# Kernel tuning notes

Hardware: AMD Instinct MI355X
Metric: run time of the kernel (lower is better)

## Reference

```python
import jax, jax.numpy as jnp
import numpy as np

B, S, D = 2, 2048, 2048
H = 16
HD = D // H  # 128


def setup_inputs() -> dict:
    key = jax.random.key(0)
    ks = jax.random.split(key, 9)
    s = 1.0 / np.sqrt(D)
    return {
        "hidden_states": jax.random.normal(ks[0], (B, S, D), dtype=jnp.float32),
        "Wq": jax.random.normal(ks[1], (D, D), dtype=jnp.float32) * s,
        "bq": jnp.zeros((D,), dtype=jnp.float32),
        "Wk": jax.random.normal(ks[2], (D, D), dtype=jnp.float32) * s,
        "bk": jnp.zeros((D,), dtype=jnp.float32),
        "Wv": jax.random.normal(ks[3], (D, D), dtype=jnp.float32) * s,
        "bv": jnp.zeros((D,), dtype=jnp.float32),
        "Wo": jax.random.normal(ks[4], (D, D), dtype=jnp.float32) * s,
        "bo": jnp.zeros((D,), dtype=jnp.float32),
    }


def reference(hidden_states, Wq, bq, Wk, bk, Wv, bv, Wo, bo):
    x = hidden_states
    # linear projections (torch Linear: x @ W.T + b)
    q = x @ Wq.T + bq
    k = x @ Wk.T + bk
    v = x @ Wv.T + bv
    # [B, S, H, HD] -> [B, H, S, HD]
    q = q.reshape(B, S, H, HD).transpose(0, 2, 1, 3)
    k = k.reshape(B, S, H, HD).transpose(0, 2, 1, 3)
    v = v.reshape(B, S, H, HD).transpose(0, 2, 1, 3)
    q = q / jnp.sqrt(jnp.float32(HD))
    # scores [B, H, S, S]
    scores = jnp.einsum("bhqd,bhkd->bhqk", q, k)
    causal = jnp.triu(jnp.full((S, S), -jnp.inf, dtype=scores.dtype), k=1)
    scores = scores + causal
    attn = jax.nn.softmax(scores, axis=-1)
    out = jnp.einsum("bhqk,bhkd->bhqd", attn, v)
    out = out.transpose(0, 2, 1, 3).reshape(B, S, D)
    return out @ Wo.T + bo
```

## Files before the change

### kernel.cpp

```cpp
#include <hip/hip_runtime.h>
#include <stdint.h>

#define S_LEN 2048
#define DMODEL 2048
#define NHEAD 16
#define HDIM 128

typedef __attribute__((ext_vector_type(8))) short short8;
typedef __attribute__((ext_vector_type(4))) float floatx4;

__device__ __forceinline__ unsigned short f2b(float f) {
  union { float f; unsigned u; } v; v.f = f;
  unsigned r = v.u + 0x7FFFu + ((v.u >> 16) & 1u);
  return (unsigned short)(r >> 16);
}

__device__ __forceinline__ void load_lds16(const unsigned short* g, unsigned short* l) {
  __builtin_amdgcn_global_load_lds((const __attribute__((address_space(1))) void*)g,
                                   (__attribute__((address_space(3))) void*)l, 16, 0, 0);
}

__global__ __launch_bounds__(256) void cvt_all(const float* __restrict__ x,
                                               const float* __restrict__ Wq, const float* __restrict__ Wk,
                                               const float* __restrict__ Wv, const float* __restrict__ Wo,
                                               unsigned short* __restrict__ xb,
                                               unsigned short* __restrict__ Wqb, unsigned short* __restrict__ Wkb,
                                               unsigned short* __restrict__ Wvb, unsigned short* __restrict__ Wob) {
  const size_t idx = (size_t)blockIdx.x * 256 + threadIdx.x;
  const int y = blockIdx.y;
  const float4* s; ushort4* d;
  if (y == 0)      { s = (const float4*)x;               d = (ushort4*)xb; }
  else if (y == 1) { s = (const float4*)x + (1u << 20);  d = (ushort4*)xb + (1u << 20); }
  else if (y == 2) { s = (const float4*)Wq;              d = (ushort4*)Wqb; }
  else if (y == 3) { s = (const float4*)Wk;              d = (ushort4*)Wkb; }
  else if (y == 4) { s = (const float4*)Wv;              d = (ushort4*)Wvb; }
  else             { s = (const float4*)Wo;              d = (ushort4*)Wob; }
  float4 f = s[idx];
  ushort4 o;
  o.x = f2b(f.x); o.y = f2b(f.y); o.z = f2b(f.z); o.w = f2b(f.w);
  d[idx] = o;
}

template <int MODE>
__global__ __launch_bounds__(256)
void gemm_bt(const unsigned short* __restrict__ A, const unsigned short* __restrict__ Bw,
             const float* __restrict__ bias, void* __restrict__ Cout,
             int M, int N, int K, float scale) {
  __shared__ unsigned short As[128 * 64];
  __shared__ unsigned short Bs[128 * 64];
  const int t = threadIdx.x;
  const int lane = t & 63, wave = t >> 6;
  const int quad = lane >> 4, lc = lane & 15;
  const int wm = wave >> 1, wn = wave & 1;
  const int m0 = blockIdx.y * 128, n0 = blockIdx.x * 128;

  const int srow = lane >> 3;
  const int skoff = ((lane & 7) ^ srow) * 8;
  const unsigned short* Ag[4];
  const unsigned short* Bg[4];
  unsigned short* Al[4];
  unsigned short* Bl[4];
#pragma unroll
  for (int i = 0; i < 4; i++) {
    int c = wave * 4 + i;
    Ag[i] = A + (size_t)(m0 + c * 8 + srow) * K + skoff;
    Bg[i] = Bw + (size_t)(n0 + c * 8 + srow) * K + skoff;
    Al[i] = &As[c * 512 + lane * 8];
    Bl[i] = &Bs[c * 512 + lane * 8];
  }

  int koff[2];
#pragma unroll
  for (int ks = 0; ks < 2; ks++) koff[ks] = ((ks * 4 + quad) ^ (lc & 7)) * 8;

  floatx4 acc[4][4] = {};

  for (int kt = 0; kt < K; kt += 64) {
    if (kt) __syncthreads();
#pragma unroll
    for (int i = 0; i < 4; i++) {
      load_lds16(Ag[i] + kt, Al[i]);
      load_lds16(Bg[i] + kt, Bl[i]);
    }
    __syncthreads();
#pragma unroll
    for (int ks = 0; ks < 2; ks++) {
      short8 av[4], bv[4];
#pragma unroll
      for (int mt = 0; mt < 4; mt++)
        av[mt] = *(const short8*)&As[(wm * 64 + mt * 16 + lc) * 64 + koff[ks]];
#pragma unroll
      for (int nt = 0; nt < 4; nt++)
        bv[nt] = *(const short8*)&Bs[(wn * 64 + nt * 16 + lc) * 64 + koff[ks]];
#pragma unroll
      for (int mt = 0; mt < 4; mt++)
#pragma unroll
        for (int nt = 0; nt < 4; nt++)
          acc[mt][nt] = __builtin_amdgcn_mfma_f32_16x16x32_bf16(av[mt], bv[nt], acc[mt][nt], 0, 0, 0);
    }
  }

#pragma unroll
  for (int nt = 0; nt < 4; nt++) {
    const int col = n0 + wn * 64 + nt * 16 + lc;
    const float bcol = bias[col];
#pragma unroll
    for (int mt = 0; mt < 4; mt++) {
      const int row0 = m0 + wm * 64 + mt * 16 + quad * 4;
      if (MODE == 1) {
        ushort4 o;
        o.x = f2b((acc[mt][nt][0] + bcol) * scale);
        o.y = f2b((acc[mt][nt][1] + bcol) * scale);
        o.z = f2b((acc[mt][nt][2] + bcol) * scale);
        o.w = f2b((acc[mt][nt][3] + bcol) * scale);
        int b = row0 >> 11;
        int s = row0 & (S_LEN - 1);
        *(ushort4*)&((unsigned short*)Cout)[((size_t)(b * DMODEL + col)) * S_LEN + s] = o;
      } else {
#pragma unroll
        for (int r = 0; r < 4; r++) {
          float v = (acc[mt][nt][r] + bcol) * scale;
          if (MODE == 2)
            ((float*)Cout)[(size_t)(row0 + r) * N + col] = v;
          else
            ((unsigned short*)Cout)[(size_t)(row0 + r) * N + col] = f2b(v);
        }
      }
    }
  }
}

__global__ __launch_bounds__(256, 2)
void attn_fwd(const unsigned short* __restrict__ Qg, const unsigned short* __restrict__ Kg,
              const unsigned short* __restrict__ Vtg, unsigned short* __restrict__ Og) {
  __shared__ unsigned short Ks[2][64 * 128];
  __shared__ unsigned short Vs[128 * 64];
  __shared__ unsigned short Ps[128 * 72];

  const int t = threadIdx.x;
  const int lane = t & 63, w = t >> 6;
  const int quad = lane >> 4, lc = lane & 15;
  const int y = blockIdx.y;
  const int tile = (y < 16) ? (int)blockIdx.x : 15 - (int)blockIdx.x;
  const int b = y >> 4, h = y & 15;
  const size_t qkbase = (size_t)b * S_LEN * DMODEL + h * HDIM;
  const size_t vtbase = ((size_t)(b * DMODEL + h * HDIM)) * S_LEN;
  const int q0 = tile * 128;
  const int wrow = q0 + w * 32;

  short8 aq[2][4];
#pragma unroll
  for (int pm = 0; pm < 2; pm++)
#pragma unroll
    for (int ks = 0; ks < 4; ks++)
      aq[pm][ks] = *(const short8*)&Qg[qkbase + (size_t)(wrow + pm * 16 + lc) * DMODEL + ks * 32 + quad * 8];

  const unsigned short* kga[4];
  const unsigned short* vga[4];
  int kloff[4], vloff[4];
#pragma unroll
  for (int i = 0; i < 4; i++) {
    int c = w * 4 + i;
    int krow = 4 * c + (lane >> 4);
    kga[i] = Kg + qkbase + (size_t)krow * DMODEL + ((lane & 15) ^ (krow & 15)) * 8;
    kloff[i] = c * 512 + lane * 8;
    int vrow = 8 * c + (lane >> 3);
    vga[i] = Vtg + vtbase + (size_t)vrow * S_LEN + ((lane & 7) ^ (vrow & 7)) * 8;
    vloff[i] = c * 512 + lane * 8;
  }

  floatx4 oaccT[8][2] = {};
  float m_run[2] = {-1e30f, -1e30f}, l_run[2] = {0.f, 0.f};

  const int kiters = 2 * tile + 2;

#pragma unroll
  for (int i = 0; i < 4; i++) load_lds16(kga[i], &Ks[0][kloff[i]]);

  for (int kb = 0; kb < kiters; kb++) {
    const int k0 = kb * 64;
    const int cur = kb & 1;
    __syncthreads();

#pragma unroll
    for (int i = 0; i < 4; i++) load_lds16(vga[i] + k0, &Vs[vloff[i]]);
    {
      const size_t knext = (size_t)((kb + 1 < kiters) ? k0 + 64 : k0) * DMODEL;
#pragma unroll
      for (int i = 0; i < 4; i++) load_lds16(kga[i] + knext, &Ks[cur ^ 1][kloff[i]]);
    }

    const bool hasw = (k0 <= wrow + 31);
    float alpha[2];
    if (hasw) {
      floatx4 st[4][2];
#pragma unroll
      for (int mt = 0; mt < 4; mt++)
#pragma unroll
        for (int pm = 0; pm < 2; pm++) st[mt][pm] = (floatx4){0.f, 0.f, 0.f, 0.f};
#pragma unroll
      for (int ks = 0; ks < 4; ks++) {
        short8 kf[4];
#pragma unroll
        for (int mt = 0; mt < 4; mt++) {
          int n = mt * 16 + lc;
          kf[mt] = *(const short8*)&Ks[cur][n * 128 + (((ks * 4 + quad) ^ (n & 15)) * 8)];
        }
#pragma unroll
        for (int mt = 0; mt < 4; mt++)
#pragma unroll
          for (int pm = 0; pm < 2; pm++)
            st[mt][pm] = __builtin_amdgcn_mfma_f32_16x16x32_bf16(kf[mt], aq[pm][ks], st[mt][pm], 0, 0, 0);
      }

      float mx[2] = {-1e30f, -1e30f};
      if (k0 + 63 > wrow) {
#pragma unroll
        for (int pm = 0; pm < 2; pm++) {
          const int qq = wrow + pm * 16 + lc;
#pragma unroll
          for (int mt = 0; mt < 4; mt++) {
            const int key = k0 + mt * 16 + quad * 4;
#pragma unroll
            for (int r = 0; r < 4; r++) {
              if (key + r > qq) st[mt][pm][r] = -1e30f;
              mx[pm] = fmaxf(mx[pm], st[mt][pm][r]);
            }
          }
        }
      } else {
#pragma unroll
        for (int pm = 0; pm < 2; pm++)
#pragma unroll
          for (int mt = 0; mt < 4; mt++)
#pragma unroll
            for (int r = 0; r < 4; r++) mx[pm] = fmaxf(mx[pm], st[mt][pm][r]);
      }
#pragma unroll
      for (int pm = 0; pm < 2; pm++) {
        mx[pm] = fmaxf(mx[pm], __shfl_xor(mx[pm], 16));
        mx[pm] = fmaxf(mx[pm], __shfl_xor(mx[pm], 32));
        float mnew = fmaxf(m_run[pm], mx[pm]);
        alpha[pm] = __builtin_amdgcn_exp2f(m_run[pm] - mnew);
        m_run[pm] = mnew;
        l_run[pm] *= alpha[pm];
      }

#pragma unroll
      for (int pm = 0; pm < 2; pm++)
#pragma unroll
        for (int mt = 0; mt < 4; mt++) {
          float p0 = __builtin_amdgcn_exp2f(st[mt][pm][0] - m_run[pm]);
          float p1 = __builtin_amdgcn_exp2f(st[mt][pm][1] - m_run[pm]);
          float p2 = __builtin_amdgcn_exp2f(st[mt][pm][2] - m_run[pm]);
          float p3 = __builtin_amdgcn_exp2f(st[mt][pm][3] - m_run[pm]);
          l_run[pm] += (p0 + p1) + (p2 + p3);
          ushort4 o;
          o.x = f2b(p0); o.y = f2b(p1); o.z = f2b(p2); o.w = f2b(p3);
          *(ushort4*)&Ps[(w * 32 + pm * 16 + lc) * 72 + mt * 16 + quad * 4] = o;
        }
    }

    asm volatile("s_waitcnt vmcnt(4)\n\ts_barrier" ::: "memory");

    if (hasw) {
#pragma unroll
      for (int mt8 = 0; mt8 < 8; mt8++)
#pragma unroll
        for (int pm = 0; pm < 2; pm++) {
          oaccT[mt8][pm][0] *= alpha[pm]; oaccT[mt8][pm][1] *= alpha[pm];
          oaccT[mt8][pm][2] *= alpha[pm]; oaccT[mt8][pm][3] *= alpha[pm];
        }

#pragma unroll
      for (int ks = 0; ks < 2; ks++) {
        short8 pf[2];
#pragma unroll
        for (int pm = 0; pm < 2; pm++)
          pf[pm] = *(const short8*)&Ps[(w * 32 + pm * 16 + lc) * 72 + ks * 32 + quad * 8];
#pragma unroll
        for (int mt8 = 0; mt8 < 8; mt8++) {
          int n = mt8 * 16 + lc;
          short8 vf = *(const short8*)&Vs[n * 64 + (((ks * 4 + quad) ^ (n & 7)) * 8)];
#pragma unroll
          for (int pm = 0; pm < 2; pm++)
            oaccT[mt8][pm] = __builtin_amdgcn_mfma_f32_16x16x32_bf16(vf, pf[pm], oaccT[mt8][pm], 0, 0, 0);
        }
      }
    }
  }

#pragma unroll
  for (int pm = 0; pm < 2; pm++) {
    l_run[pm] += __shfl_xor(l_run[pm], 16);
    l_run[pm] += __shfl_xor(l_run[pm], 32);
    float inv = 1.f / l_run[pm];
    size_t obase = ((size_t)(b * S_LEN + wrow + pm * 16 + lc)) * DMODEL + h * HDIM;
#pragma unroll
    for (int mt8 = 0; mt8 < 8; mt8++) {
      ushort4 o;
      o.x = f2b(oaccT[mt8][pm][0] * inv);
      o.y = f2b(oaccT[mt8][pm][1] * inv);
      o.z = f2b(oaccT[mt8][pm][2] * inv);
      o.w = f2b(oaccT[mt8][pm][3] * inv);
      *(ushort4*)&Og[obase + mt8 * 16 + quad * 4] = o;
    }
  }
}

extern "C" void kernel_launch(void* const* d_in, const int* in_sizes, int n_in,
                              void* d_out, int out_size, void* d_ws, size_t ws_size,
                              hipStream_t stream) {
  const float* x  = (const float*)d_in[0];
  const float* Wq = (const float*)d_in[1];
  const float* bq = (const float*)d_in[2];
  const float* Wk = (const float*)d_in[3];
  const float* bk = (const float*)d_in[4];
  const float* Wv = (const float*)d_in[5];
  const float* bv = (const float*)d_in[6];
  const float* Wo = (const float*)d_in[7];
  const float* bo = (const float*)d_in[8];

  const int M = 2 * S_LEN;
  const int N = DMODEL, K = DMODEL;

  char* w = (char*)d_ws;
  unsigned short* xb  = (unsigned short*)(w);
  unsigned short* Wqb = (unsigned short*)(w + (size_t)16 * (1 << 20));
  unsigned short* Wkb = (unsigned short*)(w + (size_t)24 * (1 << 20));
  unsigned short* Wvb = (unsigned short*)(w + (size_t)32 * (1 << 20));
  unsigned short* Wob = (unsigned short*)(w + (size_t)40 * (1 << 20));
  unsigned short* Qb  = (unsigned short*)(w + (size_t)48 * (1 << 20));
  unsigned short* Kb  = (unsigned short*)(w + (size_t)64 * (1 << 20));
  unsigned short* Vtb = (unsigned short*)(w + (size_t)80 * (1 << 20));
  unsigned short* Ob  = (unsigned short*)(w + (size_t)96 * (1 << 20));

  cvt_all<<<dim3(4096, 6), 256, 0, stream>>>(x, Wq, Wk, Wv, Wo, xb, Wqb, Wkb, Wvb, Wob);

  dim3 gg(N / 128, M / 128);
  const float qscale = 0.08838834764831843f * 1.4426950408889634f;
  gemm_bt<0><<<gg, 256, 0, stream>>>(xb, Wqb, bq, Qb, M, N, K, qscale);
  gemm_bt<0><<<gg, 256, 0, stream>>>(xb, Wkb, bk, Kb, M, N, K, 1.f);
  gemm_bt<1><<<gg, 256, 0, stream>>>(xb, Wvb, bv, Vtb, M, N, K, 1.f);

  attn_fwd<<<dim3(16, 32), 256, 0, stream>>>(Qb, Kb, Vtb, Ob);

  gemm_bt<2><<<gg, 256, 0, stream>>>(Ob, Wob, bo, d_out, M, N, K, 1.f);
}
```

Baseline: 380.8 us.

## Replace GEMMs with 256x256 pipelined LDS kernel and fuse QKV launches

Replaces the 128x128 single-buffered GEMM with a 256x256-tile, 512-thread kernel that double-buffers K slices in LDS via async global-to-LDS loads. Explicit vmcnt/lgkmcnt waits, barriers and priority hints interleave loads with MFMA clusters. The Q, K and V projections are merged into one launch selecting the weight by block index. Larger tiles raise arithmetic intensity and hide load latency, but the output GEMM now has only 128 blocks and the 128KB LDS per block limits occupancy.

```diff
diff --git a/kernel.cpp b/kernel.cpp
--- a/kernel.cpp
+++ b/kernel.cpp
@@ -41,93 +41,137 @@
   d[idx] = o;
 }
 
-template <int MODE>
-__global__ __launch_bounds__(256)
-void gemm_bt(const unsigned short* __restrict__ A, const unsigned short* __restrict__ Bw,
-             const float* __restrict__ bias, void* __restrict__ Cout,
-             int M, int N, int K, float scale) {
-  __shared__ unsigned short As[128 * 64];
-  __shared__ unsigned short Bs[128 * 64];
+
+#define REG256(buf, op, ks) (lds + ((((buf)*2 + (op)) * 2 + (ks)) * 8192))
+#define STAGE256(buf, op, ks, kt)                                                    \
+  do {                                                                               \
+    unsigned short* _d = REG256(buf, op, ks);                                        \
+    const unsigned short* _g0 = ((op) ? gB[0] : gA[0]) + (kt) * 64 + (ks) * 32;      \
+    const unsigned short* _g1 = ((op) ? gB[1] : gA[1]) + (kt) * 64 + (ks) * 32;      \
+    load_lds16(_g0, _d + ldso[0]);                                                   \
+    load_lds16(_g1, _d + ldso[1]);                                                   \
+  } while (0)
+#define RDA256(buf, ks)                                                              \
+  { _Pragma("unroll") for (int mf = 0; mf < 8; mf++)                                 \
+      av[mf] = *(const short8*)(REG256(buf, 0, ks) + aoff + mf * 512); }
+#define RDB256(buf, ks, nh)                                                          \
+  { bv[0] = *(const short8*)(REG256(buf, 1, ks) + boff + (nh) * 1024);               \
+    bv[1] = *(const short8*)(REG256(buf, 1, ks) + boff + (nh) * 1024 + 512); }
+#define MFMACL256(nh)                                                                \
+  { __builtin_amdgcn_s_setprio(1);                                                   \
+    _Pragma("unroll") for (int mf = 0; mf < 8; mf++) {                               \
+      acc[mf][(nh)*2]   = __builtin_amdgcn_mfma_f32_16x16x32_bf16(av[mf], bv[0], acc[mf][(nh)*2],   0, 0, 0); \
+      acc[mf][(nh)*2+1] = __builtin_amdgcn_mfma_f32_16x16x32_bf16(av[mf], bv[1], acc[mf][(nh)*2+1], 0, 0, 0); } \
+    __builtin_amdgcn_s_setprio(0); }
+#define BAR256 __builtin_amdgcn_s_barrier()
+#define LGKM0 do { asm volatile("s_waitcnt lgkmcnt(0)" ::: "memory"); __builtin_amdgcn_sched_barrier(0); } while (0)
+#define VMC4 asm volatile("s_waitcnt vmcnt(4)" ::: "memory")
+
+__device__ __forceinline__ void gemm256_body(const unsigned short* __restrict__ A,
+                                             const unsigned short* __restrict__ Bw,
+                                             const float* __restrict__ bias,
+                                             void* __restrict__ out, int mode, float scale,
+                                             int m0, int n0, unsigned short* lds) {
+  const int K = DMODEL;
   const int t = threadIdx.x;
-  const int lane = t & 63, wave = t >> 6;
+  const int lane = t & 63, w = t >> 6;
   const int quad = lane >> 4, lc = lane & 15;
-  const int wm = wave >> 1, wn = wave & 1;
-  const int m0 = blockIdx.y * 128, n0 = blockIdx.x * 128;
-
-  const int srow = lane >> 3;
-  const int skoff = ((lane & 7) ^ srow) * 8;
-  const unsigned short* Ag[4];
-  const unsigned short* Bg[4];
-  unsigned short* Al[4];
-  unsigned short* Bl[4];
-#pragma unroll
-  for (int i = 0; i < 4; i++) {
-    int c = wave * 4 + i;
-    Ag[i] = A + (size_t)(m0 + c * 8 + srow) * K + skoff;
-    Bg[i] = Bw + (size_t)(n0 + c * 8 + srow) * K + skoff;
-    Al[i] = &As[c * 512 + lane * 8];
-    Bl[i] = &Bs[c * 512 + lane * 8];
-  }
-
-  int koff[2];
-#pragma unroll
-  for (int ks = 0; ks < 2; ks++) koff[ks] = ((ks * 4 + quad) ^ (lc & 7)) * 8;
-
-  floatx4 acc[4][4] = {};
-
-  for (int kt = 0; kt < K; kt += 64) {
-    if (kt) __syncthreads();
-#pragma unroll
-    for (int i = 0; i < 4; i++) {
-      load_lds16(Ag[i] + kt, Al[i]);
-      load_lds16(Bg[i] + kt, Bl[i]);
-    }
-    __syncthreads();
-#pragma unroll
-    for (int ks = 0; ks < 2; ks++) {
-      short8 av[4], bv[4];
-#pragma unroll
-      for (int mt = 0; mt < 4; mt++)
-        av[mt] = *(const short8*)&As[(wm * 64 + mt * 16 + lc) * 64 + koff[ks]];
-#pragma unroll
-      for (int nt = 0; nt < 4; nt++)
-        bv[nt] = *(const short8*)&Bs[(wn * 64 + nt * 16 + lc) * 64 + koff[ks]];
-#pragma unroll
-      for (int mt = 0; mt < 4; mt++)
-#pragma unroll
-        for (int nt = 0; nt < 4; nt++)
-          acc[mt][nt] = __builtin_amdgcn_mfma_f32_16x16x32_bf16(av[mt], bv[nt], acc[mt][nt], 0, 0, 0);
-    }
-  }
-
-#pragma unroll
-  for (int nt = 0; nt < 4; nt++) {
-    const int col = n0 + wn * 64 + nt * 16 + lc;
+  const int wm = w >> 2, wn = w & 3;
+
+  const int chunkoff = ((lane & 3) ^ ((lane >> 3) & 3)) * 8;
+  const unsigned short* gA[2];
+  const unsigned short* gB[2];
+  int ldso[2];
+#pragma unroll
+  for (int i = 0; i < 2; i++) {
+    const int c = w * 2 + i;
+    const int r = c * 16 + (lane >> 2);
+    gA[i] = A + (size_t)(m0 + r) * K + chunkoff;
+    gB[i] = Bw + (size_t)(n0 + r) * K + chunkoff;
+    ldso[i] = c * 512 + lane * 8;
+  }
+
+  const int rsw = ((lc >> 1) & 3);
+  const int aoff = (wm * 128 + lc) * 32 + ((quad ^ rsw) * 8);
+  const int boff = (wn * 64 + lc) * 32 + ((quad ^ rsw) * 8);
+
+  floatx4 acc[8][4] = {};
+  short8 av[8], bv[2];
+
+  STAGE256(0, 0, 0, 0); STAGE256(0, 1, 0, 0); STAGE256(0, 0, 1, 0); STAGE256(0, 1, 1, 0);
+  STAGE256(1, 0, 0, 1); STAGE256(1, 1, 0, 1);
+  VMC4;
+  BAR256;
+
+  const int NKT = K / 64;
+  const int NIT = NKT / 2;
+  for (int it = 0; it < NIT; it++) {
+    const int kt1 = 2 * it + 1;
+    const int kt2 = (2 * it + 2 < NKT) ? 2 * it + 2 : NKT - 1;
+    const int kt3 = (2 * it + 3 < NKT) ? 2 * it + 3 : NKT - 1;
+    RDA256(0, 0); RDB256(0, 0, 0); STAGE256(1, 0, 1, kt1); BAR256; LGKM0; MFMACL256(0); BAR256;
+    RDB256(0, 0, 1);               STAGE256(1, 1, 1, kt1); BAR256; LGKM0; MFMACL256(1); BAR256;
+    RDA256(0, 1); RDB256(0, 1, 0); STAGE256(0, 0, 0, kt2); BAR256; LGKM0; MFMACL256(0); BAR256;
+    RDB256(0, 1, 1);               STAGE256(0, 1, 0, kt2); BAR256; LGKM0; MFMACL256(1); VMC4; BAR256;
+    RDA256(1, 0); RDB256(1, 0, 0); STAGE256(0, 0, 1, kt2); BAR256; LGKM0; MFMACL256(0); BAR256;
+    RDB256(1, 0, 1);               STAGE256(0, 1, 1, kt2); BAR256; LGKM0; MFMACL256(1); BAR256;
+    RDA256(1, 1); RDB256(1, 1, 0); STAGE256(1, 0, 0, kt3); BAR256; LGKM0; MFMACL256(0); BAR256;
+    RDB256(1, 1, 1);               STAGE256(1, 1, 0, kt3); BAR256; LGKM0; MFMACL256(1); VMC4; BAR256;
+  }
+
+#pragma unroll
+  for (int nf = 0; nf < 4; nf++) {
+    const int col = n0 + wn * 64 + nf * 16 + lc;
     const float bcol = bias[col];
 #pragma unroll
-    for (int mt = 0; mt < 4; mt++) {
-      const int row0 = m0 + wm * 64 + mt * 16 + quad * 4;
-      if (MODE == 1) {
+    for (int mf = 0; mf < 8; mf++) {
+      const int row0 = m0 + wm * 128 + mf * 16 + quad * 4;
+      if (mode == 1) {
         ushort4 o;
-        o.x = f2b((acc[mt][nt][0] + bcol) * scale);
-        o.y = f2b((acc[mt][nt][1] + bcol) * scale);
-        o.z = f2b((acc[mt][nt][2] + bcol) * scale);
-        o.w = f2b((acc[mt][nt][3] + bcol) * scale);
-        int b = row0 >> 11;
-        int s = row0 & (S_LEN - 1);
-        *(ushort4*)&((unsigned short*)Cout)[((size_t)(b * DMODEL + col)) * S_LEN + s] = o;
+        o.x = f2b((acc[mf][nf][0] + bcol) * scale);
+        o.y = f2b((acc[mf][nf][1] + bcol) * scale);
+        o.z = f2b((acc[mf][nf][2] + bcol) * scale);
+        o.w = f2b((acc[mf][nf][3] + bcol) * scale);
+        const int b = row0 >> 11;
+        const int s = row0 & (S_LEN - 1);
+        *(ushort4*)&((unsigned short*)out)[((size_t)(b * DMODEL + col)) * S_LEN + s] = o;
+      } else if (mode == 2) {
+#pragma unroll
+        for (int r = 0; r < 4; r++)
+          ((float*)out)[(size_t)(row0 + r) * DMODEL + col] = (acc[mf][nf][r] + bcol) * scale;
       } else {
 #pragma unroll
-        for (int r = 0; r < 4; r++) {
-          float v = (acc[mt][nt][r] + bcol) * scale;
-          if (MODE == 2)
-            ((float*)Cout)[(size_t)(row0 + r) * N + col] = v;
-          else
-            ((unsigned short*)Cout)[(size_t)(row0 + r) * N + col] = f2b(v);
-        }
-      }
-    }
-  }
+        for (int r = 0; r < 4; r++)
+          ((unsigned short*)out)[(size_t)(row0 + r) * DMODEL + col] = f2b((acc[mf][nf][r] + bcol) * scale);
+      }
+    }
+  }
+}
+
+__global__ __launch_bounds__(512, 2)
+void qkv256(const unsigned short* __restrict__ xb,
+            const unsigned short* __restrict__ Wqb, const unsigned short* __restrict__ Wkb,
+            const unsigned short* __restrict__ Wvb,
+            const float* __restrict__ bq, const float* __restrict__ bk, const float* __restrict__ bvp,
+            unsigned short* __restrict__ Qb, unsigned short* __restrict__ Kb,
+            unsigned short* __restrict__ Vtb, float qscale) {
+  __shared__ unsigned short lds[65536];
+  const int sel = blockIdx.x >> 3;
+  const int n0 = (blockIdx.x & 7) * 256;
+  const int m0 = blockIdx.y * 256;
+  const unsigned short* Bw = (sel == 0) ? Wqb : (sel == 1) ? Wkb : Wvb;
+  const float* bias = (sel == 0) ? bq : (sel == 1) ? bk : bvp;
+  void* out = (sel == 0) ? (void*)Qb : (sel == 1) ? (void*)Kb : (void*)Vtb;
+  const float scale = (sel == 0) ? qscale : 1.f;
+  const int mode = (sel == 2) ? 1 : 0;
+  gemm256_body(xb, Bw, bias, out, mode, scale, m0, n0, lds);
+}
+
+__global__ __launch_bounds__(512, 2)
+void out256(const unsigned short* __restrict__ Ob, const unsigned short* __restrict__ Wob,
+            const float* __restrict__ bo, float* __restrict__ out) {
+  __shared__ unsigned short lds[65536];
+  gemm256_body(Ob, Wob, bo, out, 2, 1.f, blockIdx.y * 256, blockIdx.x * 256, lds);
 }
 
 __global__ __launch_bounds__(256, 2)
@@ -321,9 +365,6 @@
   const float* Wo = (const float*)d_in[7];
   const float* bo = (const float*)d_in[8];
 
-  const int M = 2 * S_LEN;
-  const int N = DMODEL, K = DMODEL;
-
   char* w = (char*)d_ws;
   unsigned short* xb  = (unsigned short*)(w);
   unsigned short* Wqb = (unsigned short*)(w + (size_t)16 * (1 << 20));
@@ -337,13 +378,10 @@
 
   cvt_all<<<dim3(4096, 6), 256, 0, stream>>>(x, Wq, Wk, Wv, Wo, xb, Wqb, Wkb, Wvb, Wob);
 
-  dim3 gg(N / 128, M / 128);
   const float qscale = 0.08838834764831843f * 1.4426950408889634f;
-  gemm_bt<0><<<gg, 256, 0, stream>>>(xb, Wqb, bq, Qb, M, N, K, qscale);
-  gemm_bt<0><<<gg, 256, 0, stream>>>(xb, Wkb, bk, Kb, M, N, K, 1.f);
-  gemm_bt<1><<<gg, 256, 0, stream>>>(xb, Wvb, bv, Vtb, M, N, K, 1.f);
+  qkv256<<<dim3(24, 16), 512, 0, stream>>>(xb, Wqb, Wkb, Wvb, bq, bk, bv, Qb, Kb, Vtb, qscale);
 
   attn_fwd<<<dim3(16, 32), 256, 0, stream>>>(Qb, Kb, Vtb, Ob);
 
-  gemm_bt<2><<<gg, 256, 0, stream>>>(Ob, Wob, bo, d_out, M, N, K, 1.f);
-}
+  out256<<<dim3(8, 16), 512, 0, stream>>>(Ob, Wob, bo, (float*)d_out);
+}
```

New measurement: 395.3 us. 3.8% more time.
